# Optimization experiments

Hardware: AMD Instinct MI355X
Metric: run time of the kernel (lower is better)

The kernel has to match this reference:

```python
import jax, jax.numpy as jnp
import numpy as np

NUM_BINS = 32
SIGMA_RATIO = 1.0
SMOOTH_NR = 1e-7
SMOOTH_DR = 1e-7


def _parzen_weights(x, bin_centers, preterm):
    # x: [B, N]; returns normalized Gaussian Parzen weights [B, N, K]
    d = x[..., None] - bin_centers  # [B, N, K]
    w = jnp.exp(-preterm * d * d)
    return w / jnp.sum(w, axis=-1, keepdims=True)


def _mi_loss(pred, target):
    B = pred.shape[0]
    p = pred.reshape(B, -1)  # [B, N]
    t = target.reshape(B, -1)
    N = p.shape[1]

    # min/max are detached (.item() in torch); images in [0,1] use fixed range (0,1)
    minval = jax.lax.stop_gradient(jnp.minimum(p.min(), t.min()))
    maxval = jax.lax.stop_gradient(jnp.maximum(p.max(), t.max()))
    in_range = (maxval <= 1.0) & (minval >= 0.0)
    minval = jnp.where(in_range, jnp.float32(0.0), minval)
    maxval = jnp.where(in_range, jnp.float32(1.0), maxval)

    bin_centers = minval + (maxval - minval) * jnp.linspace(0.0, 1.0, NUM_BINS, dtype=p.dtype)  # [K]
    sigma = (maxval - minval) / (NUM_BINS - 1) * SIGMA_RATIO
    preterm = 1.0 / (2.0 * sigma * sigma)

    wa = _parzen_weights(p, bin_centers, preterm)  # [B, N, K]
    wb = _parzen_weights(t, bin_centers, preterm)  # [B, N, K]

    pa = jnp.mean(wa, axis=1)  # [B, K] == pa of shape B,1,K squeezed
    pb = jnp.mean(wb, axis=1)  # [B, K]
    pab = jnp.einsum('bnk,bnl->bkl', wa, wb) / N  # [B, K, K] joint histogram
    papb = pa[:, :, None] * pb[:, None, :]  # [B, K, K] outer product == bmm(pa^T, pb)

    mi = jnp.sum(pab * jnp.log((pab + SMOOTH_NR) / (papb + SMOOTH_DR) + SMOOTH_DR), axis=(-1, -2))  # [B]
    return -jnp.mean(mi)  # reduction='mean', negated


def setup_inputs() -> dict:
    key = jax.random.key(0)
    k1, k2 = jax.random.split(key)
    shape = (1, 1, 128, 128, 128)
    pred = jax.random.uniform(k1, shape, dtype=jnp.float32)
    target = jax.random.uniform(k2, shape, dtype=jnp.float32)
    return {"pred": pred, "target": target}


def reference(pred, target):
    return _mi_loss(pred, target)
```

## Files before the change

### kernel.cpp

```cpp
#include <hip/hip_runtime.h>
#include <math.h>

#ifndef __has_builtin
#define __has_builtin(x) 0
#endif
#if __has_builtin(__builtin_amdgcn_exp2f)
#define EXP2F(x) __builtin_amdgcn_exp2f(x)
#else
#define EXP2F(x) exp2f(x)
#endif
#if __has_builtin(__builtin_amdgcn_rcpf)
#define RCPF(x) __builtin_amdgcn_rcpf(x)
#else
#define RCPF(x) (1.0f / (x))
#endif

typedef _Float16 f16x8 __attribute__((ext_vector_type(8)));
typedef _Float16 h2 __attribute__((ext_vector_type(2)));
typedef float f32x4 __attribute__((ext_vector_type(4)));

union Frag {
  f16x8 v;
  h2 p[4];
  _Float16 e[8];
};

__device__ __forceinline__ h2 pkrtz(float a, float b) {
#if __has_builtin(__builtin_amdgcn_cvt_pkrtz)
  return __builtin_bit_cast(h2, __builtin_amdgcn_cvt_pkrtz(a, b));
#else
  h2 r; r.x = (_Float16)a; r.y = (_Float16)b; return r;
#endif
}

constexpr int KBINS = 32;
constexpr int MM_BLOCKS = 512;
constexpr int MAIN_BLOCKS = 1024;
constexpr int NTHR = 512;
constexpr int WPB = 8;
constexpr int BATCH = 32;
constexpr int NSLOT = 8;
constexpr int ACC_OFF_F = 4096;

#define MFMA16(a, b, c) __builtin_amdgcn_mfma_f32_16x16x32_f16((a), (b), (c), 0, 0, 0)

template <int CTRL>
__device__ __forceinline__ float rot_add(float v) {
  int r = __builtin_amdgcn_update_dpp(0, __builtin_bit_cast(int, v), CTRL, 0xF, 0xF, true);
  return v + __builtin_bit_cast(float, r);
}
__device__ __forceinline__ float row_sum16(float v) {
  v = rot_add<0x128>(v);
  v = rot_add<0x124>(v);
  v = rot_add<0x122>(v);
  v = rot_add<0x121>(v);
  return v;
}

__device__ __forceinline__ void eraw(float x, float c0, float c1, float npl2,
                                     float& e0, float& e1, float& s) {
  float d0 = x - c0, d1 = x - c1;
  e0 = EXP2F((npl2 * d0) * d0);
  e1 = EXP2F((npl2 * d1) * d1);
  s = row_sum16(e0 + e1);
}

__global__ __launch_bounds__(256) void k_minmax(const float* __restrict__ p,
                                                const float* __restrict__ t,
                                                int n, float* __restrict__ ws) {
  int tid = blockIdx.x * 256 + threadIdx.x;
  int nth = gridDim.x * 256;
  if (tid < NSLOT * 1024) ((double*)(ws + ACC_OFF_F))[tid] = 0.0;

  float mn = INFINITY, mx = -INFINITY;
  int n4 = n >> 2;
  const float4* p4 = (const float4*)p;
  const float4* t4 = (const float4*)t;
  for (int i = tid; i < n4; i += nth) {
    float4 a = p4[i];
    mn = fminf(mn, fminf(fminf(a.x, a.y), fminf(a.z, a.w)));
    mx = fmaxf(mx, fmaxf(fmaxf(a.x, a.y), fmaxf(a.z, a.w)));
    float4 b = t4[i];
    mn = fminf(mn, fminf(fminf(b.x, b.y), fminf(b.z, b.w)));
    mx = fmaxf(mx, fmaxf(fmaxf(b.x, b.y), fmaxf(b.z, b.w)));
  }
  for (int i = (n4 << 2) + tid; i < n; i += nth) {
    mn = fminf(mn, fminf(p[i], t[i]));
    mx = fmaxf(mx, fmaxf(p[i], t[i]));
  }
  for (int off = 32; off; off >>= 1) {
    mn = fminf(mn, __shfl_xor(mn, off, 64));
    mx = fmaxf(mx, __shfl_xor(mx, off, 64));
  }
  __shared__ float smn[4], smx[4];
  int wv = threadIdx.x >> 6;
  if ((threadIdx.x & 63) == 0) { smn[wv] = mn; smx[wv] = mx; }
  __syncthreads();
  if (threadIdx.x == 0) {
    mn = fminf(fminf(smn[0], smn[1]), fminf(smn[2], smn[3]));
    mx = fmaxf(fmaxf(smx[0], smx[1]), fmaxf(smx[2], smx[3]));
    ws[16 + 2 * blockIdx.x] = mn;
    ws[17 + 2 * blockIdx.x] = mx;
  }
}

__global__ __launch_bounds__(NTHR, 4) void k_main(const float* __restrict__ p,
                                                  const float* __restrict__ t,
                                                  int n, float* __restrict__ ws) {
  __shared__ __align__(16) float red[WPB][KBINS * KBINS];
  __shared__ float s_par[4];

  const int tidx = threadIdx.x;
  const int lane = tidx & 63;
  const int wv = tidx >> 6;

  if (tidx < 64) {
    float mn = INFINITY, mx = -INFINITY;
    for (int b = lane; b < MM_BLOCKS; b += 64) {
      mn = fminf(mn, ws[16 + 2 * b]);
      mx = fmaxf(mx, ws[17 + 2 * b]);
    }
    for (int off = 32; off; off >>= 1) {
      mn = fminf(mn, __shfl_xor(mn, off, 64));
      mx = fmaxf(mx, __shfl_xor(mx, off, 64));
    }
    if (lane == 0) {
      bool in_range = (mx <= 1.0f) && (mn >= 0.0f);
      float minv = in_range ? 0.0f : mn;
      float maxv = in_range ? 1.0f : mx;
      float drange = maxv - minv;
      float sigma = drange * (1.0f / (KBINS - 1));
      float preterm = 1.0f / (2.0f * sigma * sigma);
      s_par[0] = minv;
      s_par[1] = drange * (1.0f / (KBINS - 1));
      s_par[2] = preterm * 1.44269504088896340736f;
    }
  }
  __syncthreads();
  const float minv = s_par[0], delta = s_par[1];
  const float npl2 = -s_par[2];

  const int m = lane & 15;
  const int quad = lane >> 4;
  const int qb = quad << 3;
  const float c0 = fmaf(delta, (float)m, minv);
  const float c1 = fmaf(delta, (float)(m + 16), minv);

  f32x4 acc00 = {0.f, 0.f, 0.f, 0.f};
  f32x4 acc01 = {0.f, 0.f, 0.f, 0.f};
  f32x4 acc10 = {0.f, 0.f, 0.f, 0.f};
  f32x4 acc11 = {0.f, 0.f, 0.f, 0.f};

  const int per_wave = n >> 13;
  const int base = (blockIdx.x * WPB + wv) * per_wave;

  for (int it = 0; it < per_wave; it += BATCH) {
    const int sbase = base + it + qb;
    float4 a0 = *(const float4*)(p + sbase);
    float4 a1 = *(const float4*)(p + sbase + 4);
    float4 b0 = *(const float4*)(t + sbase);
    float4 b1 = *(const float4*)(t + sbase + 4);
    float xa[8] = {a0.x, a0.y, a0.z, a0.w, a1.x, a1.y, a1.z, a1.w};
    float xb[8] = {b0.x, b0.y, b0.z, b0.w, b1.x, b1.y, b1.z, b1.w};

    Frag Ah0, Al0, Ah1, Al1, Bh0, Bl0, Bh1, Bl1;
#pragma unroll
    for (int jp = 0; jp < 4; ++jp) {
      float ea00, ea01, sa0, ea10, ea11, sa1;
      float eb00, eb01, sb0, eb10, eb11, sb1;
      eraw(xa[2 * jp],     c0, c1, npl2, ea00, ea01, sa0);
      eraw(xa[2 * jp + 1], c0, c1, npl2, ea10, ea11, sa1);
      eraw(xb[2 * jp],     c0, c1, npl2, eb00, eb01, sb0);
      eraw(xb[2 * jp + 1], c0, c1, npl2, eb10, eb11, sb1);
      float pr0 = sa0 * sb0;
      float i0 = RCPF(pr0);
      i0 = i0 * fmaf(-pr0, i0, 2.0f);
      i0 *= 4096.0f;
      float pr1 = sa1 * sb1;
      float i1 = RCPF(pr1);
      i1 = i1 * fmaf(-pr1, i1, 2.0f);
      i1 *= 4096.0f;
      float wa00 = ea00 * i0, wa01 = ea01 * i0;
      float wa10 = ea10 * i1, wa11 = ea11 * i1;
      float wb00 = eb00 * 64.0f, wb01 = eb01 * 64.0f;
      float wb10 = eb10 * 64.0f, wb11 = eb11 * 64.0f;
      h2 ha0 = pkrtz(wa00, wa10);
      h2 ha1 = pkrtz(wa01, wa11);
      h2 hb0 = pkrtz(wb00, wb10);
      h2 hb1 = pkrtz(wb01, wb11);
      Ah0.p[jp] = ha0; Ah1.p[jp] = ha1;
      Bh0.p[jp] = hb0; Bh1.p[jp] = hb1;
      Al0.e[2 * jp]     = (_Float16)(wa00 - (float)ha0.x);
      Al0.e[2 * jp + 1] = (_Float16)(wa10 - (float)ha0.y);
      Al1.e[2 * jp]     = (_Float16)(wa01 - (float)ha1.x);
      Al1.e[2 * jp + 1] = (_Float16)(wa11 - (float)ha1.y);
      Bl0.e[2 * jp]     = (_Float16)(wb00 - (float)hb0.x);
      Bl0.e[2 * jp + 1] = (_Float16)(wb10 - (float)hb0.y);
      Bl1.e[2 * jp]     = (_Float16)(wb01 - (float)hb1.x);
      Bl1.e[2 * jp + 1] = (_Float16)(wb11 - (float)hb1.y);
    }
    acc00 = MFMA16(Ah0.v, Bh0.v, acc00);
    acc01 = MFMA16(Ah0.v, Bh1.v, acc01);
    acc10 = MFMA16(Ah1.v, Bh0.v, acc10);
    acc11 = MFMA16(Ah1.v, Bh1.v, acc11);
    acc00 = MFMA16(Al0.v, Bh0.v, acc00);
    acc01 = MFMA16(Al0.v, Bh1.v, acc01);
    acc10 = MFMA16(Al1.v, Bh0.v, acc10);
    acc11 = MFMA16(Al1.v, Bh1.v, acc11);
    acc00 = MFMA16(Ah0.v, Bl0.v, acc00);
    acc01 = MFMA16(Ah0.v, Bl1.v, acc01);
    acc10 = MFMA16(Ah1.v, Bl0.v, acc10);
    acc11 = MFMA16(Ah1.v, Bl1.v, acc11);
    acc00 = MFMA16(Al0.v, Bl0.v, acc00);
    acc01 = MFMA16(Al0.v, Bl1.v, acc01);
    acc10 = MFMA16(Al1.v, Bl0.v, acc10);
    acc11 = MFMA16(Al1.v, Bl1.v, acc11);
  }

#pragma unroll
  for (int reg = 0; reg < 4; ++reg) {
    int r0 = quad * 4 + reg;
    red[wv][r0 * KBINS + m] = acc00[reg];
    red[wv][r0 * KBINS + 16 + m] = acc01[reg];
    red[wv][(16 + r0) * KBINS + m] = acc10[reg];
    red[wv][(16 + r0) * KBINS + 16 + m] = acc11[reg];
  }
  __syncthreads();
  {
    int c = 2 * tidx;
    float s0 = 0.f, s1 = 0.f;
#pragma unroll
    for (int w = 0; w < WPB; ++w) {
      float2 v = *(const float2*)&red[w][c];
      s0 += v.x;
      s1 += v.y;
    }
    double* acc = (double*)(ws + ACC_OFF_F) + (size_t)(blockIdx.x & (NSLOT - 1)) * 1024;
    unsafeAtomicAdd(&acc[c], (double)s0);
    unsafeAtomicAdd(&acc[c + 1], (double)s1);
  }
}

__global__ __launch_bounds__(1024) void k_final(const float* __restrict__ ws_f,
                                                float* __restrict__ out, int n) {
  const double* acc = (const double*)(ws_f + ACC_OFF_F);
  __shared__ double pab_s[1024];
  __shared__ double pa_s[32], pb_s[32];
  __shared__ double wsum[16];
  int tid = threadIdx.x;
  double s = 0.0;
#pragma unroll
  for (int slot = 0; slot < NSLOT; ++slot) s += acc[(size_t)slot * 1024 + tid];
  double pab = s / ((double)n * 262144.0);
  pab_s[tid] = pab;
  __syncthreads();
  if (tid < 32) {
    double a = 0.0;
    for (int l = 0; l < 32; ++l) a += pab_s[tid * 32 + l];
    pa_s[tid] = a;
  } else if (tid < 64) {
    int l = tid - 32;
    double b = 0.0;
    for (int k2 = 0; k2 < 32; ++k2) b += pab_s[k2 * 32 + l];
    pb_s[l] = b;
  }
  __syncthreads();
  int k = tid >> 5, l = tid & 31;
  double papb = pa_s[k] * pb_s[l];
  double v = pab * log((pab + 1e-7) / (papb + 1e-7) + 1e-7);
  for (int off = 32; off; off >>= 1) v += __shfl_down(v, off, 64);
  if ((tid & 63) == 0) wsum[tid >> 6] = v;
  __syncthreads();
  if (tid < 64) {
    double w = (tid < 16) ? wsum[tid] : 0.0;
    for (int off = 8; off; off >>= 1) w += __shfl_down(w, off, 64);
    if (tid == 0) out[0] = (float)(-w);
  }
}

extern "C" void kernel_launch(void* const* d_in, const int* in_sizes, int n_in,
                              void* d_out, int out_size, void* d_ws, size_t ws_size,
                              hipStream_t stream) {
  const float* p = (const float*)d_in[0];
  const float* t = (const float*)d_in[1];
  float* out = (float*)d_out;
  float* ws = (float*)d_ws;
  int n = in_sizes[0];

  k_minmax<<<dim3(MM_BLOCKS), dim3(256), 0, stream>>>(p, t, n, ws);
  k_main<<<dim3(MAIN_BLOCKS), dim3(NTHR), 0, stream>>>(p, t, n, ws);
  k_final<<<dim3(1), dim3(1024), 0, stream>>>(ws, out, n);
}
```

Baseline: 128.6 us.

## Prefetch next inputs, cheapen hi/lo fp16 split, widen atomic slot count

Loads the next batch of pred/target values before computing the current batch, so global-load latency overlaps the exp and MFMA work. The hi/lo fp16 split now truncates the hi part by masking mantissa bits instead of converting to fp16 and back, which saves conversions per weight. Atomic accumulation is spread over 64 double slots instead of 8 to reduce contention, and the final kernel sums them with four independent accumulators. This costs more registers for the prefetch, more workspace memory, and more reads in the final kernel.

```diff
diff --git a/kernel.cpp b/kernel.cpp
--- a/kernel.cpp
+++ b/kernel.cpp
@@ -22,7 +22,6 @@
 union Frag {
   f16x8 v;
   h2 p[4];
-  _Float16 e[8];
 };
 
 __device__ __forceinline__ h2 pkrtz(float a, float b) {
@@ -33,13 +32,17 @@
 #endif
 }
 
+__device__ __forceinline__ float trunc16(float w) {
+  return __builtin_bit_cast(float, __builtin_bit_cast(unsigned int, w) & 0xFFFFE000u);
+}
+
 constexpr int KBINS = 32;
 constexpr int MM_BLOCKS = 512;
 constexpr int MAIN_BLOCKS = 1024;
 constexpr int NTHR = 512;
 constexpr int WPB = 8;
 constexpr int BATCH = 32;
-constexpr int NSLOT = 8;
+constexpr int NSLOT = 64;
 constexpr int ACC_OFF_F = 4096;
 
 #define MFMA16(a, b, c) __builtin_amdgcn_mfma_f32_16x16x32_f16((a), (b), (c), 0, 0, 0)
@@ -154,14 +157,21 @@
   const int per_wave = n >> 13;
   const int base = (blockIdx.x * WPB + wv) * per_wave;
 
+  float4 a0 = *(const float4*)(p + base + qb);
+  float4 a1 = *(const float4*)(p + base + qb + 4);
+  float4 b0 = *(const float4*)(t + base + qb);
+  float4 b1 = *(const float4*)(t + base + qb + 4);
+
   for (int it = 0; it < per_wave; it += BATCH) {
-    const int sbase = base + it + qb;
-    float4 a0 = *(const float4*)(p + sbase);
-    float4 a1 = *(const float4*)(p + sbase + 4);
-    float4 b0 = *(const float4*)(t + sbase);
-    float4 b1 = *(const float4*)(t + sbase + 4);
     float xa[8] = {a0.x, a0.y, a0.z, a0.w, a1.x, a1.y, a1.z, a1.w};
     float xb[8] = {b0.x, b0.y, b0.z, b0.w, b1.x, b1.y, b1.z, b1.w};
+    if (it + BATCH < per_wave) {
+      const int nbase = base + it + BATCH + qb;
+      a0 = *(const float4*)(p + nbase);
+      a1 = *(const float4*)(p + nbase + 4);
+      b0 = *(const float4*)(t + nbase);
+      b1 = *(const float4*)(t + nbase + 4);
+    }
 
     Frag Ah0, Al0, Ah1, Al1, Bh0, Bl0, Bh1, Bl1;
 #pragma unroll
@@ -184,20 +194,23 @@
       float wa10 = ea10 * i1, wa11 = ea11 * i1;
       float wb00 = eb00 * 64.0f, wb01 = eb01 * 64.0f;
       float wb10 = eb10 * 64.0f, wb11 = eb11 * 64.0f;
-      h2 ha0 = pkrtz(wa00, wa10);
-      h2 ha1 = pkrtz(wa01, wa11);
-      h2 hb0 = pkrtz(wb00, wb10);
-      h2 hb1 = pkrtz(wb01, wb11);
-      Ah0.p[jp] = ha0; Ah1.p[jp] = ha1;
-      Bh0.p[jp] = hb0; Bh1.p[jp] = hb1;
-      Al0.e[2 * jp]     = (_Float16)(wa00 - (float)ha0.x);
-      Al0.e[2 * jp + 1] = (_Float16)(wa10 - (float)ha0.y);
-      Al1.e[2 * jp]     = (_Float16)(wa01 - (float)ha1.x);
-      Al1.e[2 * jp + 1] = (_Float16)(wa11 - (float)ha1.y);
-      Bl0.e[2 * jp]     = (_Float16)(wb00 - (float)hb0.x);
-      Bl0.e[2 * jp + 1] = (_Float16)(wb10 - (float)hb0.y);
-      Bl1.e[2 * jp]     = (_Float16)(wb01 - (float)hb1.x);
-      Bl1.e[2 * jp + 1] = (_Float16)(wb11 - (float)hb1.y);
+      float H;
+      H = trunc16(wa00); float la00 = wa00 - H; float ha00 = H;
+      H = trunc16(wa10); float la10 = wa10 - H; float ha10 = H;
+      H = trunc16(wa01); float la01 = wa01 - H; float ha01 = H;
+      H = trunc16(wa11); float la11 = wa11 - H; float ha11 = H;
+      H = trunc16(wb00); float lb00 = wb00 - H; float hb00 = H;
+      H = trunc16(wb10); float lb10 = wb10 - H; float hb10 = H;
+      H = trunc16(wb01); float lb01 = wb01 - H; float hb01 = H;
+      H = trunc16(wb11); float lb11 = wb11 - H; float hb11 = H;
+      Ah0.p[jp] = pkrtz(ha00, ha10);
+      Ah1.p[jp] = pkrtz(ha01, ha11);
+      Bh0.p[jp] = pkrtz(hb00, hb10);
+      Bh1.p[jp] = pkrtz(hb01, hb11);
+      Al0.p[jp] = h2{(_Float16)la00, (_Float16)la10};
+      Al1.p[jp] = h2{(_Float16)la01, (_Float16)la11};
+      Bl0.p[jp] = h2{(_Float16)lb00, (_Float16)lb10};
+      Bl1.p[jp] = h2{(_Float16)lb01, (_Float16)lb11};
     }
     acc00 = MFMA16(Ah0.v, Bh0.v, acc00);
     acc01 = MFMA16(Ah0.v, Bh1.v, acc01);
@@ -248,9 +261,15 @@
   __shared__ double pa_s[32], pb_s[32];
   __shared__ double wsum[16];
   int tid = threadIdx.x;
-  double s = 0.0;
+  double s0 = 0.0, s1 = 0.0, s2 = 0.0, s3 = 0.0;
 #pragma unroll
-  for (int slot = 0; slot < NSLOT; ++slot) s += acc[(size_t)slot * 1024 + tid];
+  for (int slot = 0; slot < NSLOT; slot += 4) {
+    s0 += acc[(size_t)(slot + 0) * 1024 + tid];
+    s1 += acc[(size_t)(slot + 1) * 1024 + tid];
+    s2 += acc[(size_t)(slot + 2) * 1024 + tid];
+    s3 += acc[(size_t)(slot + 3) * 1024 + tid];
+  }
+  double s = (s0 + s1) + (s2 + s3);
   double pab = s / ((double)n * 262144.0);
   pab_s[tid] = pab;
   __syncthreads();
```

New measurement: 131.8 us. 2.5% more time.
